# Optimization experiments

Hardware: AMD Instinct MI355X
Metric: run time of the kernel (lower is better)

Reference implementation:

```python
import jax, jax.numpy as jnp
import numpy as np

B, C, D, H, W = 2, 512, 32, 32, 32
L, CTX = 256, 768
NH, HD, G = 8, 64, 8
EPS = 1e-5


def group_norm(x, w, b):
    Bb, Cc, Dd, Hh, Ww = x.shape
    xg = x.reshape(Bb, G, Cc // G, Dd, Hh, Ww)
    mu = xg.mean(axis=(2, 3, 4, 5), keepdims=True)
    var = xg.var(axis=(2, 3, 4, 5), keepdims=True)
    xn = ((xg - mu) * jax.lax.rsqrt(var + EPS)).reshape(Bb, Cc, Dd, Hh, Ww)
    return xn * w[None, :, None, None, None] + b[None, :, None, None, None]


def layer_norm(x, w, b):
    mu = x.mean(axis=-1, keepdims=True)
    var = x.var(axis=-1, keepdims=True)
    return (x - mu) * jax.lax.rsqrt(var + EPS) * w + b


def setup_inputs() -> dict:
    key = jax.random.key(0)
    ks = jax.random.split(key, 8)
    s = 0.02  # weight init scale
    return {
        "x": jax.random.normal(ks[0], (B, C, D, H, W), jnp.float32),
        "context": jax.random.normal(ks[1], (B, L, CTX), jnp.float32),
        "gn_w": jnp.ones((C,), jnp.float32),
        "gn_b": jnp.zeros((C,), jnp.float32),
        "ln_w": jnp.ones((CTX,), jnp.float32),
        "ln_b": jnp.zeros((CTX,), jnp.float32),
        "q_w": jax.random.normal(ks[2], (C, C), jnp.float32) * s,
        "q_b": jnp.zeros((C,), jnp.float32),
        "k_w": jax.random.normal(ks[3], (C, CTX), jnp.float32) * s,
        "k_b": jnp.zeros((C,), jnp.float32),
        "v_w": jax.random.normal(ks[4], (C, CTX), jnp.float32) * s,
        "v_b": jnp.zeros((C,), jnp.float32),
        "proj_w": jax.random.normal(ks[5], (C, C), jnp.float32) * s,
        "proj_b": jnp.zeros((C,), jnp.float32),
    }


def reference(x, context, gn_w, gn_b, ln_w, ln_b, q_w, q_b, k_w, k_b, v_w, v_b, proj_w, proj_b):
    Bb, Cc, Dd, Hh, Ww = x.shape
    S = Dd * Hh * Ww
    h = group_norm(x, gn_w, gn_b)
    ctx = layer_norm(context, ln_w, ln_b)
    # 1x1 Conv3d == per-voxel linear over channels
    q = jnp.einsum('oc,bcdhw->bodhw', q_w, h) + q_b[None, :, None, None, None]
    q = q.reshape(Bb, NH, HD, S)                                        # (b,h,e,s)
    k = (ctx @ k_w.T + k_b).reshape(Bb, L, NH, HD).transpose(0, 2, 1, 3)  # (b,h,l,e)
    v = (ctx @ v_w.T + v_b).reshape(Bb, L, NH, HD).transpose(0, 2, 1, 3)  # (b,h,l,e)
    scale = HD ** -0.5
    attn = jnp.einsum('bhes,bhle->bhsl', q, k) * scale                  # (b,h,S,L)
    attn = jax.nn.softmax(attn, axis=-1)
    out = jnp.einsum('bhsl,bhle->bhes', attn, v).reshape(Bb, Cc, Dd, Hh, Ww)
    out = jnp.einsum('oc,bcdhw->bodhw', proj_w, out) + proj_b[None, :, None, None, None]
    return out + x
```

## Files before the change

kernel.cpp:

```cpp
#include <hip/hip_runtime.h>

typedef unsigned short u16;
typedef unsigned int u32;
typedef __attribute__((ext_vector_type(4))) float f32x4;
typedef __attribute__((ext_vector_type(8))) short bf16x8;
typedef __attribute__((ext_vector_type(8))) u16 u16x8;
typedef __attribute__((ext_vector_type(4))) u16 u16x4;
typedef __attribute__((ext_vector_type(4))) u32 u32x4;

#define DEVI __device__ __forceinline__

constexpr int C_ = 512, S_ = 32768, L_ = 256, CTX_ = 768;

DEVI u16 f2b(float f) {
    union { float f; unsigned u; } x; x.f = f;
    unsigned r = x.u + 0x7fffu + ((x.u >> 16) & 1u);
    return (u16)(r >> 16);
}

DEVI f32x4 mfma16(bf16x8 a, bf16x8 b, f32x4 c) {
    return __builtin_amdgcn_mfma_f32_16x16x32_bf16(a, b, c, 0, 0, 0);
}

DEVI void gload16(const void* g, void* l) {
    __builtin_amdgcn_global_load_lds(
        (const __attribute__((address_space(1))) void*)g,
        (__attribute__((address_space(3))) void*)l, 16, 0, 0);
}

DEVI u32 cvtpk(float lo, float hi) {
    u32 d;
    asm("v_cvt_pk_bf16_f32 %0, %1, %2" : "=v"(d) : "v"(lo), "v"(hi));
    return d;
}
DEVI void pl32(u32& a, u32& b) {
    asm volatile("v_permlane32_swap_b32 %0, %1" : "+v"(a), "+v"(b));
}
DEVI void pl16(u32& a, u32& b) {
    asm volatile("v_permlane16_swap_b32 %0, %1" : "+v"(a), "+v"(b));
}

__global__ __launch_bounds__(256) void cvt_w(
    const float* __restrict__ a0, const float* __restrict__ a1,
    const float* __restrict__ a2, const float* __restrict__ a3,
    u16* __restrict__ o0, u16* __restrict__ o1,
    u16* __restrict__ o2, u16* __restrict__ o3)
{
    int which = blockIdx.y;
    const float* src = which == 0 ? a0 : which == 1 ? a1 : which == 2 ? a2 : a3;
    u16* dst = which == 0 ? o0 : which == 1 ? o1 : which == 2 ? o2 : o3;
    int n4 = (which == 1 || which == 2) ? (512 * 768 / 4) : (512 * 512 / 4);
    int i = blockIdx.x * 256 + threadIdx.x;
    if (i < n4) {
        float4 v = ((const float4*)src)[i];
        u16x4 o; o[0] = f2b(v.x); o[1] = f2b(v.y); o[2] = f2b(v.z); o[3] = f2b(v.w);
        ((u16x4*)dst)[i] = o;
    }
}

__global__ __launch_bounds__(256) void gn_partial(const float* __restrict__ x,
                                                  float* __restrict__ part)
{
    const int bg = blockIdx.y, blk = blockIdx.x, tid = threadIdx.x;
    const float* base = x + (size_t)bg * 64 * S_ + (size_t)blk * 512;
    float s1 = 0.f, s2 = 0.f;
    for (int c = 0; c < 64; ++c) {
        const float* row = base + (size_t)c * S_;
        float v0 = row[tid], v1 = row[tid + 256];
        s1 += v0 + v1; s2 += v0 * v0 + v1 * v1;
    }
    for (int m = 1; m < 64; m <<= 1) { s1 += __shfl_xor(s1, m); s2 += __shfl_xor(s2, m); }
    __shared__ float a1[4], a2[4];
    int w = tid >> 6, lane = tid & 63;
    if (lane == 0) { a1[w] = s1; a2[w] = s2; }
    __syncthreads();
    if (tid == 0) {
        part[(bg * 64 + blk) * 2 + 0] = a1[0] + a1[1] + a1[2] + a1[3];
        part[(bg * 64 + blk) * 2 + 1] = a2[0] + a2[1] + a2[2] + a2[3];
    }
}

__global__ __launch_bounds__(64) void gn_final(const float* __restrict__ part,
                                               float* __restrict__ stats)
{
    int bg = blockIdx.x, tid = threadIdx.x;
    float s1 = part[(bg * 64 + tid) * 2], s2 = part[(bg * 64 + tid) * 2 + 1];
    for (int m = 1; m < 64; m <<= 1) { s1 += __shfl_xor(s1, m); s2 += __shfl_xor(s2, m); }
    if (tid == 0) {
        const float invN = 1.0f / (64.0f * (float)S_);
        float mu = s1 * invN, var = s2 * invN - mu * mu;
        stats[bg * 2] = mu;
        stats[bg * 2 + 1] = rsqrtf(var + 1e-5f);
    }
}

__global__ __launch_bounds__(256) void gn_apply(
    const float* __restrict__ x, const float* __restrict__ stats,
    const float* __restrict__ gw, const float* __restrict__ gb,
    u16* __restrict__ ht)
{
    __shared__ float tile[64][65];
    const int tid = threadIdx.x, sl = tid & 63, c4 = tid >> 6;
    const int s0 = blockIdx.x * 64, c0 = blockIdx.y * 64, b = blockIdx.z;
    const int bg = b * 8 + (c0 >> 6);
    const float mu = stats[bg * 2], rstd = stats[bg * 2 + 1];
#pragma unroll
    for (int i = 0; i < 16; ++i) {
        int cl = c4 * 16 + i;
        float wv = gw[c0 + cl], bv = gb[c0 + cl];
        float v = x[((size_t)(b * C_ + c0 + cl)) * S_ + s0 + sl];
        tile[sl][cl] = (v - mu) * rstd * wv + bv;
    }
    __syncthreads();
#pragma unroll
    for (int i = 0; i < 16; ++i) {
        int so = c4 * 16 + i;
        ht[((size_t)(b * S_ + s0 + so)) * C_ + c0 + sl] = f2b(tile[so][sl]);
    }
}

__global__ __launch_bounds__(256) void ln_ctx(
    const float* __restrict__ ctx, const float* __restrict__ lw,
    const float* __restrict__ lb, u16* __restrict__ cn)
{
    const int row = blockIdx.x, tid = threadIdx.x;
    const float* p = ctx + (size_t)row * CTX_;
    float v0 = p[tid], v1 = p[tid + 256], v2 = p[tid + 512];
    float s1 = v0 + v1 + v2, s2 = v0 * v0 + v1 * v1 + v2 * v2;
    for (int m = 1; m < 64; m <<= 1) { s1 += __shfl_xor(s1, m); s2 += __shfl_xor(s2, m); }
    __shared__ float a1[4], a2[4];
    int w = tid >> 6, lane = tid & 63;
    if (lane == 0) { a1[w] = s1; a2[w] = s2; }
    __syncthreads();
    s1 = a1[0] + a1[1] + a1[2] + a1[3];
    s2 = a2[0] + a2[1] + a2[2] + a2[3];
    const float invN = 1.0f / 768.0f;
    float mu = s1 * invN, rstd = rsqrtf(s2 * invN - mu * mu + 1e-5f);
    u16* o = cn + (size_t)row * CTX_;
    o[tid]       = f2b((v0 - mu) * rstd * lw[tid]       + lb[tid]);
    o[tid + 256] = f2b((v1 - mu) * rstd * lw[tid + 256] + lb[tid + 256]);
    o[tid + 512] = f2b((v2 - mu) * rstd * lw[tid + 512] + lb[tid + 512]);
}

template <int MODE>
__global__ __launch_bounds__(256, 2) void gemm_nt(
    const u16* __restrict__ A, const u16* __restrict__ Bp,
    const float* __restrict__ bias, void* __restrict__ outp,
    const float* __restrict__ resid, int K, int ldo,
    size_t aStride, size_t bStride, size_t oStride, float scale,
    const u16* __restrict__ Bp2, const float* __restrict__ bias2,
    void* __restrict__ outp2)
{
    __shared__ __align__(16) u16 lA[4][4096];
    __shared__ __align__(16) u16 lB[4][4096];
    const int tid = threadIdx.x;
    const int w = tid >> 6, lane = tid & 63;
    const int g = lane >> 4, r = lane & 15;
    const int m0 = blockIdx.x * 128, n0 = blockIdx.y * 128;
    const int z = blockIdx.z;
    A += (size_t)z * aStride;
    const u16* Bsel = Bp;
    if constexpr (MODE == 3) { if (z) Bsel = Bp2; }
    Bsel += (size_t)z * bStride;

    const int l8 = lane & 7, lh = lane >> 3;
    const int u_ = l8 ^ lh;
    const int mro = (lh << 1) + (u_ >> 2);
    const int kco = (u_ & 3) * 8;
    const int wr = w >> 1, wc = w & 1;
    const int nt = K >> 5;

    f32x4 acc[4][4];
#pragma unroll
    for (int m = 0; m < 4; ++m)
#pragma unroll
        for (int n = 0; n < 4; ++n) acc[m][n] = f32x4{0.f, 0.f, 0.f, 0.f};

#define STAGE_T(t) {                                                           \
    int bi_ = (t) & 3;                                                         \
    size_t ko_ = (size_t)((t) * 32 + kco);                                     \
    _Pragma("unroll")                                                          \
    for (int j = 0; j < 2; ++j) {                                              \
        int grow_ = w * 32 + j * 16 + mro;                                     \
        gload16(A + (size_t)(m0 + grow_) * K + ko_,                            \
                &lA[bi_][(w * 16 + j * 8) << 6]);                              \
        gload16(Bsel + (size_t)(n0 + grow_) * K + ko_,                         \
                &lB[bi_][(w * 16 + j * 8) << 6]);                              \
    } }

    STAGE_T(0); STAGE_T(1); STAGE_T(2);

    for (int t = 0; t < nt; ++t) {
        asm volatile("s_waitcnt lgkmcnt(0)" ::: "memory");
        if (t < nt - 2)      asm volatile("s_waitcnt vmcnt(8)" ::: "memory");
        else if (t == nt - 2) asm volatile("s_waitcnt vmcnt(4)" ::: "memory");
        else                  asm volatile("s_waitcnt vmcnt(0)" ::: "memory");
        __builtin_amdgcn_s_barrier();
        asm volatile("" ::: "memory");
        const int bi = t & 3;
        bf16x8 af[4], bf_[4];
#pragma unroll
        for (int m = 0; m < 4; ++m) {
            int row = wr * 32 + m * 8 + (r >> 1);
            int slot = (((r & 1) << 2) + g) ^ ((r >> 1) & 7);
            af[m] = *(const bf16x8*)&lA[bi][(row << 6) + (slot << 3)];
        }
#pragma unroll
        for (int n = 0; n < 4; ++n) {
            int row = wc * 32 + n * 8 + (r >> 1);
            int slot = (((r & 1) << 2) + g) ^ ((r >> 1) & 7);
            bf_[n] = *(const bf16x8*)&lB[bi][(row << 6) + (slot << 3)];
        }
        if (t + 3 < nt) STAGE_T(t + 3);
#pragma unroll
        for (int m = 0; m < 4; ++m)
#pragma unroll
            for (int n = 0; n < 4; ++n)
                acc[m][n] = mfma16(af[m], bf_[n], acc[m][n]);
    }
#undef STAGE_T

    if constexpr (MODE == 0) {
        u16* ob = (u16*)outp + (size_t)z * oStride;
#pragma unroll
        for (int n = 0; n < 4; ++n) {
            int gn = n0 + wc * 64 + n * 16 + r;
            float bn = bias[gn] * scale;
#pragma unroll
            for (int m = 0; m < 4; ++m) {
                int gm = m0 + wr * 64 + m * 16 + g * 4;
#pragma unroll
                for (int i = 0; i < 4; ++i)
                    ob[(size_t)(gm + i) * ldo + gn] = f2b(acc[m][n][i] * scale + bn);
            }
        }
    } else if constexpr (MODE == 2) {
        float* of = (float*)outp + (size_t)z * oStride;
        const float* rs = resid + (size_t)z * oStride;
#pragma unroll
        for (int m = 0; m < 4; ++m) {
            int gm = m0 + wr * 64 + m * 16 + g * 4;
#pragma unroll
            for (int i = 0; i < 4; ++i) {
                float bm = bias[gm + i];
#pragma unroll
                for (int n = 0; n < 4; ++n) {
                    int gn = n0 + wc * 64 + n * 16 + r;
                    size_t idx = (size_t)(gm + i) * ldo + gn;
                    of[idx] = acc[m][n][i] + bm + rs[idx];
                }
            }
        }
    } else if constexpr (MODE == 3) {
        if (z == 0) {
            u16* ob = (u16*)outp;
#pragma unroll
            for (int n = 0; n < 4; ++n) {
                int gn = n0 + wc * 64 + n * 16 + r;
                float bn = bias[gn];
#pragma unroll
                for (int m = 0; m < 4; ++m) {
                    int gm = m0 + wr * 64 + m * 16 + g * 4;
#pragma unroll
                    for (int i = 0; i < 4; ++i)
                        ob[(size_t)(gm + i) * ldo + gn] = f2b(acc[m][n][i] + bn);
                }
            }
        } else {
            u16* ob = (u16*)outp2;
#pragma unroll
            for (int n = 0; n < 4; ++n) {
                int gn = n0 + wc * 64 + n * 16 + r;
                float bn = bias2[gn];
#pragma unroll
                for (int m = 0; m < 4; ++m) {
                    int gm = m0 + wr * 64 + m * 16 + g * 4;
                    int bb = gm >> 8, l = gm & 255;
                    u16x4 pk;
#pragma unroll
                    for (int i = 0; i < 4; ++i) pk[i] = f2b(acc[m][n][i] + bn);
                    *(u16x4*)&ob[((size_t)(bb * 512 + gn)) * 256 + l] = pk;
                }
            }
        }
    }
}

__global__ __launch_bounds__(256, 2) void attn_kernel(
    const u16* __restrict__ q, const u16* __restrict__ kk,
    const u16* __restrict__ vv, u16* __restrict__ ao)
{
    __shared__ __align__(16) u16 sm[32768];
    const int tid = threadIdx.x;
    const int w = tid >> 6, lane = tid & 63;
    const int g = lane >> 4, r = lane & 15;
    const int bh = blockIdx.y, b = bh >> 3, h = bh & 7;
    const int s0 = blockIdx.x * 128;

    {
        const u16* kbase = kk + ((size_t)b * L_) * C_ + h * 64;
#pragma unroll
        for (int j = 0; j < 8; ++j) {
            int idx = j * 256 + tid;
            int l = idx >> 3, ch = idx & 7;
            u16x8 val = *(const u16x8*)(kbase + (size_t)l * C_ + ch * 8);
            *(u16x8*)&sm[l * 64 + ((ch ^ (l & 7)) << 3)] = val;
        }
        const u16* vbase = vv + ((size_t)bh * 64) * 256;
#pragma unroll
        for (int j = 0; j < 8; ++j) {
            int idx = j * 256 + tid;
            int e = idx >> 5, ch = idx & 31;
            u16x8 val = *(const u16x8*)(vbase + (size_t)e * 256 + ch * 8);
            *(u16x8*)&sm[16384 + e * 256 + ((ch ^ (e & 7)) << 3)] = val;
        }
    }

    const int sw = s0 + w * 32;
    bf16x8 qf[2][2];
#pragma unroll
    for (int m = 0; m < 2; ++m)
#pragma unroll
        for (int kt = 0; kt < 2; ++kt)
            qf[m][kt] = *(const bf16x8*)(q + ((size_t)(b * S_ + sw + m * 16 + r)) * C_
                                         + h * 64 + kt * 32 + g * 8);
    __syncthreads();

    f32x4 accs[2][16];
#pragma unroll
    for (int m = 0; m < 2; ++m)
#pragma unroll
        for (int n = 0; n < 16; ++n) accs[m][n] = f32x4{0.f, 0.f, 0.f, 0.f};
    __builtin_amdgcn_s_setprio(1);
#pragma unroll
    for (int n = 0; n < 16; ++n) {
#pragma unroll
        for (int kt = 0; kt < 2; ++kt) {
            int c = kt * 4 + g;
            bf16x8 kf = *(const bf16x8*)&sm[(n * 16 + r) * 64 + ((c ^ (r & 7)) << 3)];
#pragma unroll
            for (int m = 0; m < 2; ++m) accs[m][n] = mfma16(kf, qf[m][kt], accs[m][n]);
        }
    }
    __builtin_amdgcn_s_setprio(0);

    float inv[2];
#pragma unroll
    for (int m = 0; m < 2; ++m) {
        float mx = accs[m][0][0];
#pragma unroll
        for (int n = 0; n < 16; ++n)
#pragma unroll
            for (int i = 0; i < 4; ++i) mx = fmaxf(mx, accs[m][n][i]);
        mx = fmaxf(mx, __shfl_xor(mx, 16));
        mx = fmaxf(mx, __shfl_xor(mx, 32));
        float sum = 0.f;
#pragma unroll
        for (int n = 0; n < 16; ++n)
#pragma unroll
            for (int i = 0; i < 4; ++i) {
                float e = __expf(accs[m][n][i] - mx);
                accs[m][n][i] = e; sum += e;
            }
        sum += __shfl_xor(sum, 16);
        sum += __shfl_xor(sum, 32);
        inv[m] = 1.0f / sum;
    }

    f32x4 acco[2][4];
#pragma unroll
    for (int m = 0; m < 2; ++m)
#pragma unroll
        for (int n = 0; n < 4; ++n) acco[m][n] = f32x4{0.f, 0.f, 0.f, 0.f};

#pragma unroll
    for (int c = 0; c < 8; ++c) {
        bf16x8 pa[2];
#pragma unroll
        for (int m = 0; m < 2; ++m) {
            u32 x0 = cvtpk(accs[m][2 * c][0] * inv[m], accs[m][2 * c][1] * inv[m]);
            u32 x1 = cvtpk(accs[m][2 * c][2] * inv[m], accs[m][2 * c][3] * inv[m]);
            u32 y0 = cvtpk(accs[m][2 * c + 1][0] * inv[m], accs[m][2 * c + 1][1] * inv[m]);
            u32 y1 = cvtpk(accs[m][2 * c + 1][2] * inv[m], accs[m][2 * c + 1][3] * inv[m]);
            pl32(x0, y0);
            pl32(x1, y1);
            pl16(x0, y0);
            pl16(x1, y1);
            u32x4 pw; pw[0] = x0; pw[1] = x1; pw[2] = y0; pw[3] = y1;
            pa[m] = *(bf16x8*)&pw;
        }
        bf16x8 vf[4];
#pragma unroll
        for (int n = 0; n < 4; ++n) {
            int e = n * 16 + r;
            vf[n] = *(const bf16x8*)&sm[16384 + e * 256 + (((c * 4 + g) ^ (r & 7)) << 3)];
        }
        __builtin_amdgcn_s_setprio(1);
#pragma unroll
        for (int m = 0; m < 2; ++m)
#pragma unroll
            for (int n = 0; n < 4; ++n)
                acco[m][n] = mfma16(pa[m], vf[n], acco[m][n]);
        __builtin_amdgcn_s_setprio(0);
    }

#pragma unroll
    for (int m = 0; m < 2; ++m)
#pragma unroll
        for (int n = 0; n < 4; ++n)
#pragma unroll
            for (int i = 0; i < 4; ++i) {
                int s = sw + m * 16 + g * 4 + i;
                int e = n * 16 + r;
                ao[((size_t)(b * S_ + s)) * C_ + h * 64 + e] = f2b(acco[m][n][i]);
            }
}

extern "C" void kernel_launch(void* const* d_in, const int* in_sizes, int n_in,
                              void* d_out, int out_size, void* d_ws, size_t ws_size,
                              hipStream_t stream)
{
    (void)in_sizes; (void)n_in; (void)out_size; (void)ws_size;
    const float* x    = (const float*)d_in[0];
    const float* ctx  = (const float*)d_in[1];
    const float* gn_w = (const float*)d_in[2];
    const float* gn_b = (const float*)d_in[3];
    const float* ln_w = (const float*)d_in[4];
    const float* ln_b = (const float*)d_in[5];
    const float* q_w  = (const float*)d_in[6];
    const float* q_b  = (const float*)d_in[7];
    const float* k_w  = (const float*)d_in[8];
    const float* k_b  = (const float*)d_in[9];
    const float* v_w  = (const float*)d_in[10];
    const float* v_b  = (const float*)d_in[11];
    const float* p_w  = (const float*)d_in[12];
    const float* p_b  = (const float*)d_in[13];
    float* out = (float*)d_out;

    char* ws = (char*)d_ws;
    constexpr size_t WS_WQ   = 0;
    constexpr size_t WS_WK   = WS_WQ + (size_t)512 * 512 * 2;
    constexpr size_t WS_WV   = WS_WK + (size_t)512 * 768 * 2;
    constexpr size_t WS_WP   = WS_WV + (size_t)512 * 768 * 2;
    constexpr size_t WS_PART = WS_WP + (size_t)512 * 512 * 2;
    constexpr size_t WS_STAT = WS_PART + (size_t)16 * 64 * 2 * 4;
    constexpr size_t WS_CTXN = WS_STAT + 256;
    constexpr size_t WS_K    = WS_CTXN + (size_t)512 * 768 * 2;
    constexpr size_t WS_V    = WS_K + (size_t)2 * 8 * 256 * 64 * 2;
    constexpr size_t WS_Q    = WS_V + (size_t)2 * 8 * 256 * 64 * 2;
    constexpr size_t WS_H    = WS_Q + (size_t)2 * 32768 * 512 * 2;

    u16* wq = (u16*)(ws + WS_WQ);
    u16* wk = (u16*)(ws + WS_WK);
    u16* wv = (u16*)(ws + WS_WV);
    u16* wp = (u16*)(ws + WS_WP);
    float* part  = (float*)(ws + WS_PART);
    float* stats = (float*)(ws + WS_STAT);
    u16* ctxn = (u16*)(ws + WS_CTXN);
    u16* kt   = (u16*)(ws + WS_K);
    u16* vt   = (u16*)(ws + WS_V);
    u16* qt   = (u16*)(ws + WS_Q);
    u16* ht   = (u16*)(ws + WS_H);
    u16* ao   = ht;

    const size_t bsc = (size_t)S_ * C_;

    cvt_w<<<dim3(384, 4), 256, 0, stream>>>(q_w, k_w, v_w, p_w, wq, wk, wv, wp);
    gn_partial<<<dim3(64, 16), 256, 0, stream>>>(x, part);
    gn_final<<<16, 64, 0, stream>>>(part, stats);
    gn_apply<<<dim3(512, 8, 2), 256, 0, stream>>>(x, stats, gn_w, gn_b, ht);
    ln_ctx<<<512, 256, 0, stream>>>(ctx, ln_w, ln_b, ctxn);
    gemm_nt<0><<<dim3(256, 4, 2), 256, 0, stream>>>(ht, wq, q_b, qt, nullptr,
                                                    512, 512, bsc, 0, bsc, 0.125f,
                                                    nullptr, nullptr, nullptr);
    gemm_nt<3><<<dim3(4, 4, 2), 256, 0, stream>>>(ctxn, wk, k_b, kt, nullptr,
                                                  768, 512, 0, 0, 0, 1.0f,
                                                  wv, v_b, vt);
    attn_kernel<<<dim3(256, 16), 256, 0, stream>>>(qt, kt, vt, ao);
    gemm_nt<2><<<dim3(4, 256, 2), 256, 0, stream>>>(wp, ao, p_b, out, x,
                                                    512, S_, 0, bsc, bsc, 1.0f,
                                                    nullptr, nullptr, nullptr);
}
```

Before: 285.8 us.

## Double-buffer GEMM with block swizzle, higher occupancy, and vectorize GN partial

The GEMM's 4-stage LDS ring with manual vmcnt waits becomes a simpler 2-stage double buffer synchronized by __syncthreads. LDS per block is halved and launch bounds go to 4 blocks per CU to raise occupancy. Block indices are remapped through an 8-way swizzle, with a SWAP option so the Q projection walks N fastest. The group-norm partial reduction now reads float4 with half as many blocks. The shallower prefetch and the extra barrier per k-step may expose global load latency that the deeper pipeline used to hide.

```diff
diff --git a/kernel.cpp b/kernel.cpp
--- a/kernel.cpp
+++ b/kernel.cpp
@@ -62,12 +62,12 @@
                                                   float* __restrict__ part)
 {
     const int bg = blockIdx.y, blk = blockIdx.x, tid = threadIdx.x;
-    const float* base = x + (size_t)bg * 64 * S_ + (size_t)blk * 512;
+    const float* base = x + (size_t)bg * 64 * S_ + (size_t)blk * 1024 + tid * 4;
     float s1 = 0.f, s2 = 0.f;
     for (int c = 0; c < 64; ++c) {
-        const float* row = base + (size_t)c * S_;
-        float v0 = row[tid], v1 = row[tid + 256];
-        s1 += v0 + v1; s2 += v0 * v0 + v1 * v1;
+        float4 v = *(const float4*)(base + (size_t)c * S_);
+        s1 += v.x + v.y + v.z + v.w;
+        s2 += v.x * v.x + v.y * v.y + v.z * v.z + v.w * v.w;
     }
     for (int m = 1; m < 64; m <<= 1) { s1 += __shfl_xor(s1, m); s2 += __shfl_xor(s2, m); }
     __shared__ float a1[4], a2[4];
@@ -75,8 +75,8 @@
     if (lane == 0) { a1[w] = s1; a2[w] = s2; }
     __syncthreads();
     if (tid == 0) {
-        part[(bg * 64 + blk) * 2 + 0] = a1[0] + a1[1] + a1[2] + a1[3];
-        part[(bg * 64 + blk) * 2 + 1] = a2[0] + a2[1] + a2[2] + a2[3];
+        part[(bg * 32 + blk) * 2 + 0] = a1[0] + a1[1] + a1[2] + a1[3];
+        part[(bg * 32 + blk) * 2 + 1] = a2[0] + a2[1] + a2[2] + a2[3];
     }
 }
 
@@ -84,8 +84,9 @@
                                                float* __restrict__ stats)
 {
     int bg = blockIdx.x, tid = threadIdx.x;
-    float s1 = part[(bg * 64 + tid) * 2], s2 = part[(bg * 64 + tid) * 2 + 1];
-    for (int m = 1; m < 64; m <<= 1) { s1 += __shfl_xor(s1, m); s2 += __shfl_xor(s2, m); }
+    float s1 = tid < 32 ? part[(bg * 32 + tid) * 2] : 0.f;
+    float s2 = tid < 32 ? part[(bg * 32 + tid) * 2 + 1] : 0.f;
+    for (int m = 1; m < 32; m <<= 1) { s1 += __shfl_xor(s1, m); s2 += __shfl_xor(s2, m); }
     if (tid == 0) {
         const float invN = 1.0f / (64.0f * (float)S_);
         float mu = s1 * invN, var = s2 * invN - mu * mu;
@@ -142,8 +143,8 @@
     o[tid + 512] = f2b((v2 - mu) * rstd * lw[tid + 512] + lb[tid + 512]);
 }
 
-template <int MODE>
-__global__ __launch_bounds__(256, 2) void gemm_nt(
+template <int MODE, bool SWAP>
+__global__ __launch_bounds__(256, 4) void gemm_nt(
     const u16* __restrict__ A, const u16* __restrict__ Bp,
     const float* __restrict__ bias, void* __restrict__ outp,
     const float* __restrict__ resid, int K, int ldo,
@@ -151,12 +152,17 @@
     const u16* __restrict__ Bp2, const float* __restrict__ bias2,
     void* __restrict__ outp2)
 {
-    __shared__ __align__(16) u16 lA[4][4096];
-    __shared__ __align__(16) u16 lB[4][4096];
+    __shared__ __align__(16) u16 lA[2][4096];
+    __shared__ __align__(16) u16 lB[2][4096];
     const int tid = threadIdx.x;
     const int w = tid >> 6, lane = tid & 63;
     const int g = lane >> 4, r = lane & 15;
-    const int m0 = blockIdx.x * 128, n0 = blockIdx.y * 128;
+
+    const int nx = gridDim.x, nxy = nx * gridDim.y;
+    const int raw = blockIdx.x + nx * blockIdx.y;
+    const int tile = (raw & 7) * (nxy >> 3) + (raw >> 3);
+    const int bx = tile % nx, by = tile / nx;
+    const int m0 = (SWAP ? by : bx) * 128, n0 = (SWAP ? bx : by) * 128;
     const int z = blockIdx.z;
     A += (size_t)z * aStride;
     const u16* Bsel = Bp;
@@ -176,8 +182,7 @@
 #pragma unroll
         for (int n = 0; n < 4; ++n) acc[m][n] = f32x4{0.f, 0.f, 0.f, 0.f};
 
-#define STAGE_T(t) {                                                           \
-    int bi_ = (t) & 3;                                                         \
+#define STAGE_T(t, bi_) {                                                      \
     size_t ko_ = (size_t)((t) * 32 + kco);                                     \
     _Pragma("unroll")                                                          \
     for (int j = 0; j < 2; ++j) {                                              \
@@ -188,35 +193,31 @@
                 &lB[bi_][(w * 16 + j * 8) << 6]);                              \
     } }
 
-    STAGE_T(0); STAGE_T(1); STAGE_T(2);
+    STAGE_T(0, 0);
+    __syncthreads();
 
     for (int t = 0; t < nt; ++t) {
-        asm volatile("s_waitcnt lgkmcnt(0)" ::: "memory");
-        if (t < nt - 2)      asm volatile("s_waitcnt vmcnt(8)" ::: "memory");
-        else if (t == nt - 2) asm volatile("s_waitcnt vmcnt(4)" ::: "memory");
-        else                  asm volatile("s_waitcnt vmcnt(0)" ::: "memory");
-        __builtin_amdgcn_s_barrier();
-        asm volatile("" ::: "memory");
-        const int bi = t & 3;
+        const int cur = t & 1;
+        if (t + 1 < nt) STAGE_T(t + 1, cur ^ 1);
         bf16x8 af[4], bf_[4];
 #pragma unroll
         for (int m = 0; m < 4; ++m) {
             int row = wr * 32 + m * 8 + (r >> 1);
             int slot = (((r & 1) << 2) + g) ^ ((r >> 1) & 7);
-            af[m] = *(const bf16x8*)&lA[bi][(row << 6) + (slot << 3)];
+            af[m] = *(const bf16x8*)&lA[cur][(row << 6) + (slot << 3)];
         }
 #pragma unroll
         for (int n = 0; n < 4; ++n) {
             int row = wc * 32 + n * 8 + (r >> 1);
             int slot = (((r & 1) << 2) + g) ^ ((r >> 1) & 7);
-            bf_[n] = *(const bf16x8*)&lB[bi][(row << 6) + (slot << 3)];
-        }
-        if (t + 3 < nt) STAGE_T(t + 3);
+            bf_[n] = *(const bf16x8*)&lB[cur][(row << 6) + (slot << 3)];
+        }
 #pragma unroll
         for (int m = 0; m < 4; ++m)
 #pragma unroll
             for (int n = 0; n < 4; ++n)
                 acc[m][n] = mfma16(af[m], bf_[n], acc[m][n]);
+        __syncthreads();
     }
 #undef STAGE_T
 
@@ -466,18 +467,18 @@
     const size_t bsc = (size_t)S_ * C_;
 
     cvt_w<<<dim3(384, 4), 256, 0, stream>>>(q_w, k_w, v_w, p_w, wq, wk, wv, wp);
-    gn_partial<<<dim3(64, 16), 256, 0, stream>>>(x, part);
+    gn_partial<<<dim3(32, 16), 256, 0, stream>>>(x, part);
     gn_final<<<16, 64, 0, stream>>>(part, stats);
     gn_apply<<<dim3(512, 8, 2), 256, 0, stream>>>(x, stats, gn_w, gn_b, ht);
     ln_ctx<<<512, 256, 0, stream>>>(ctx, ln_w, ln_b, ctxn);
-    gemm_nt<0><<<dim3(256, 4, 2), 256, 0, stream>>>(ht, wq, q_b, qt, nullptr,
-                                                    512, 512, bsc, 0, bsc, 0.125f,
-                                                    nullptr, nullptr, nullptr);
-    gemm_nt<3><<<dim3(4, 4, 2), 256, 0, stream>>>(ctxn, wk, k_b, kt, nullptr,
-                                                  768, 512, 0, 0, 0, 1.0f,
-                                                  wv, v_b, vt);
+    gemm_nt<0, true><<<dim3(4, 256, 2), 256, 0, stream>>>(
+        ht, wq, q_b, qt, nullptr, 512, 512, bsc, 0, bsc, 0.125f,
+        nullptr, nullptr, nullptr);
+    gemm_nt<3, false><<<dim3(4, 4, 2), 256, 0, stream>>>(
+        ctxn, wk, k_b, kt, nullptr, 768, 512, 0, 0, 0, 1.0f,
+        wv, v_b, vt);
     attn_kernel<<<dim3(256, 16), 256, 0, stream>>>(qt, kt, vt, ao);
-    gemm_nt<2><<<dim3(4, 256, 2), 256, 0, stream>>>(wp, ao, p_b, out, x,
-                                                    512, S_, 0, bsc, bsc, 1.0f,
-                                                    nullptr, nullptr, nullptr);
-}
+    gemm_nt<2, false><<<dim3(4, 256, 2), 256, 0, stream>>>(
+        wp, ao, p_b, out, x, 512, S_, 0, bsc, bsc, 1.0f,
+        nullptr, nullptr, nullptr);
+}
```

Result: faster. 279.5 us (-2.2%).
